# Kernel tuning notes

Measured on AMD Instinct MI355X. Metric: run time of the kernel, lower is better.

Reference implementation:

```python
import jax, jax.numpy as jnp
import numpy as np

N_EMBED = 1024
N_HEADS = 16
HEAD_SIZE = N_EMBED // N_HEADS
B, T = 4, 2048
LN_EPS = 1e-5


def _layer_norm(x, gamma, beta):
    mu = jnp.mean(x, axis=-1, keepdims=True)
    var = jnp.var(x, axis=-1, keepdims=True)
    return (x - mu) * jax.lax.rsqrt(var + LN_EPS) * gamma + beta


def setup_inputs() -> dict:
    key = jax.random.key(0)
    ks = jax.random.split(key, 12)
    s = 1.0 / np.sqrt(N_EMBED)
    sh = 1.0 / np.sqrt(4 * N_EMBED)
    return {
        "x": jax.random.normal(ks[0], (B, T, N_EMBED), jnp.float32),
        "Wk": jax.random.uniform(ks[1], (N_EMBED, N_EMBED), jnp.float32, -s, s),
        "Wq": jax.random.uniform(ks[2], (N_EMBED, N_EMBED), jnp.float32, -s, s),
        "Wv": jax.random.uniform(ks[3], (N_EMBED, N_EMBED), jnp.float32, -s, s),
        "Wproj": jax.random.uniform(ks[4], (N_EMBED, N_EMBED), jnp.float32, -s, s),
        "bproj": jax.random.uniform(ks[5], (N_EMBED,), jnp.float32, -s, s),
        "W1": jax.random.uniform(ks[6], (N_EMBED, 4 * N_EMBED), jnp.float32, -s, s),
        "b1": jax.random.uniform(ks[7], (4 * N_EMBED,), jnp.float32, -s, s),
        "W2": jax.random.uniform(ks[8], (4 * N_EMBED, N_EMBED), jnp.float32, -sh, sh),
        "b2": jax.random.uniform(ks[9], (N_EMBED,), jnp.float32, -sh, sh),
        "g1": jnp.ones((N_EMBED,), jnp.float32),
        "beta1": jnp.zeros((N_EMBED,), jnp.float32),
        "g2": jnp.ones((N_EMBED,), jnp.float32),
        "beta2": jnp.zeros((N_EMBED,), jnp.float32),
    }


def reference(x, Wk, Wq, Wv, Wproj, bproj, W1, b1, W2, b2, g1, beta1, g2, beta2):
    Bt, Tt, C = x.shape
    h = _layer_norm(x, g1, beta1)
    # project and split heads: (B, H, T, D)
    def heads(W):
        return (h @ W).reshape(Bt, Tt, N_HEADS, HEAD_SIZE).transpose(0, 2, 1, 3)
    q, k, v = heads(Wq), heads(Wk), heads(Wv)
    wei = jnp.einsum("bhtd,bhsd->bhts", q, k) / np.sqrt(HEAD_SIZE)
    causal = jnp.tril(jnp.ones((Tt, Tt), bool))
    wei = jnp.where(causal, wei, -jnp.inf)
    wei = jax.nn.softmax(wei, axis=-1)
    out = jnp.einsum("bhts,bhsd->bhtd", wei, v)
    out = out.transpose(0, 2, 1, 3).reshape(Bt, Tt, C)
    x = x + out @ Wproj + bproj
    h2 = _layer_norm(x, g2, beta2)
    ff = jax.nn.relu(h2 @ W1 + b1) @ W2 + b2
    return x + ff
```

## Files before the change

### kernel.cpp

```cpp
#include <hip/hip_runtime.h>
#include <stdint.h>

typedef __bf16 bf16x8 __attribute__((ext_vector_type(8)));
typedef float f32x4 __attribute__((ext_vector_type(4)));
typedef unsigned short u16x8 __attribute__((ext_vector_type(8)));
typedef unsigned short u16x4 __attribute__((ext_vector_type(4)));
typedef unsigned int u32x2 __attribute__((ext_vector_type(2)));
typedef float fvec4 __attribute__((ext_vector_type(4)));

__device__ __forceinline__ unsigned short f2b(float f) {
  unsigned u = __builtin_bit_cast(unsigned, f);
  return (unsigned short)((u + 0x7fffu + ((u >> 16) & 1u)) >> 16);
}

__device__ __forceinline__ bf16x8 ldfrag(const unsigned short* p) {
  return __builtin_bit_cast(bf16x8, *(const u16x8*)p);
}

__device__ __forceinline__ float fexp2(float x) {
  float r;
  asm("v_exp_f32 %0, %1" : "=v"(r) : "v"(x));
  return r;
}

__device__ __forceinline__ unsigned cvtpk(float a, float b) {
  unsigned r;
  asm("v_cvt_pk_bf16_f32 %0, %1, %2" : "=v"(r) : "v"(a), "v"(b));
  return r;
}

__device__ __forceinline__ void gload_lds16(const void* g, void* l) {
  auto gp = reinterpret_cast<const __attribute__((address_space(1))) void*>(
      reinterpret_cast<uintptr_t>(g));
  auto lp = reinterpret_cast<__attribute__((address_space(3))) void*>(
      reinterpret_cast<uintptr_t>(l));
  __builtin_amdgcn_global_load_lds(gp, lp, 16, 0, 0);
}

__global__ void transpose_cast(const float* __restrict__ W, unsigned short* __restrict__ Wt,
                               int K, int N) {
  __shared__ float tile[32][33];
  const int n0 = blockIdx.x * 32, k0 = blockIdx.y * 32;
  const int tx = threadIdx.x, ty = threadIdx.y;
#pragma unroll
  for (int j = 0; j < 4; ++j)
    tile[ty + j * 8][tx] = W[(size_t)(k0 + ty + j * 8) * N + n0 + tx];
  __syncthreads();
#pragma unroll
  for (int j = 0; j < 4; ++j)
    Wt[(size_t)(n0 + ty + j * 8) * K + k0 + tx] = f2b(tile[tx][ty + j * 8]);
}

__global__ void ln_kernel(const float* __restrict__ X, const float* __restrict__ g,
                          const float* __restrict__ be, unsigned short* __restrict__ H) {
  const int row = (blockIdx.x * blockDim.x + threadIdx.x) >> 6;
  const int l = threadIdx.x & 63;
  const float* xr = X + (size_t)row * 1024;
  fvec4 v[4];
  float s = 0.f, sq = 0.f;
#pragma unroll
  for (int i = 0; i < 4; ++i) {
    v[i] = *(const fvec4*)(xr + i * 256 + l * 4);
#pragma unroll
    for (int j = 0; j < 4; ++j) { s += v[i][j]; sq += v[i][j] * v[i][j]; }
  }
#pragma unroll
  for (int off = 32; off >= 1; off >>= 1) {
    s += __shfl_xor(s, off);
    sq += __shfl_xor(sq, off);
  }
  const float mean = s * (1.f / 1024.f);
  const float var = sq * (1.f / 1024.f) - mean * mean;
  const float rstd = rsqrtf(var + 1e-5f);
#pragma unroll
  for (int i = 0; i < 4; ++i) {
    const int col = i * 256 + l * 4;
    fvec4 gg = *(const fvec4*)(g + col);
    fvec4 bb = *(const fvec4*)(be + col);
    u16x4 o;
#pragma unroll
    for (int j = 0; j < 4; ++j) o[j] = f2b((v[i][j] - mean) * rstd * gg[j] + bb[j]);
    *(u16x4*)(H + (size_t)row * 1024 + col) = o;
  }
}

template <int BM, int BN, int WM, int WN, int NBUF, int NTH, int EPI>
__global__ __launch_bounds__(NTH, 2) void gemm8p(
    const unsigned short* __restrict__ A, const unsigned short* __restrict__ Bt,
    const float* __restrict__ bias, const float* __restrict__ resid,
    float* __restrict__ Cf, unsigned short* __restrict__ Cb,
    unsigned short* __restrict__ pK, unsigned short* __restrict__ pVT,
    int M, int N, int K, int ntiles) {
  constexpr int BK = 32;
  constexpr int ASZ = BM * BK * 2;
  constexpr int BSZ = BN * BK * 2;
  constexpr int BUFSZ = ASZ + BSZ;
  constexpr int NW = NTH / 64;
  static_assert(WM * WN == NW, "wave grid");
  constexpr int MF = BM / (WM * 16);
  constexpr int NF = BN / (WN * 16);
  constexpr int UA = ASZ / (NTH * 16);
  constexpr int UB = BSZ / (NTH * 16);
  constexpr int UNITS = UA + UB;
  constexpr int VMSTEADY = (NBUF - 2) * UNITS;
  static_assert(UA * NTH * 16 == ASZ && UB * NTH * 16 == BSZ, "unit split");
  __shared__ __align__(16) char lds[NBUF * BUFSZ];

  const int tid = threadIdx.x;
  const int w = tid >> 6, l = tid & 63;
  const int wr = w / WN, wc = w % WN;
  const int kg = l >> 4, fr = l & 15;
  const int xtiles = N / BN;
  const int nblk = (int)gridDim.x;

  int Aoff[MF], Boff[NF];
#pragma unroll
  for (int m = 0; m < MF; ++m) {
    const int r = wr * (MF * 16) + m * 16 + fr;
    Aoff[m] = r * 64 + ((kg * 16) ^ (((r >> 1) & 3) << 4));
  }
#pragma unroll
  for (int n = 0; n < NF; ++n) {
    const int r = wc * (NF * 16) + n * 16 + fr;
    Boff[n] = ASZ + r * 64 + ((kg * 16) ^ (((r >> 1) & 3) << 4));
  }

  for (int tl = (int)blockIdx.x; tl < ntiles; tl += nblk) {
    if (tl != (int)blockIdx.x) __builtin_amdgcn_s_barrier();
    const int q8 = ntiles >> 3;
    const int swz = (tl & 7) * q8 + (tl >> 3);
    const size_t am0 = (size_t)(swz / xtiles) * BM;
    const size_t bn0 = (size_t)(swz % xtiles) * BN;

    const char* src[UNITS];
#pragma unroll
    for (int u = 0; u < UA; ++u) {
      const int flatq = u * NTH + tid;
      const int row = flatq >> 2;
      const int scb = ((flatq & 3) << 4) ^ (((row >> 1) & 3) << 4);
      src[u] = (const char*)(A + (am0 + row) * K) + scb;
    }
#pragma unroll
    for (int u = 0; u < UB; ++u) {
      const int flatq = u * NTH + tid;
      const int row = flatq >> 2;
      const int scb = ((flatq & 3) << 4) ^ (((row >> 1) & 3) << 4);
      src[UA + u] = (const char*)(Bt + (bn0 + row) * K) + scb;
    }

    f32x4 acc[MF][NF];
#pragma unroll
    for (int m = 0; m < MF; ++m)
#pragma unroll
      for (int n = 0; n < NF; ++n) acc[m][n] = (f32x4){0.f, 0.f, 0.f, 0.f};

    auto stage = [&](int sb) {
#pragma unroll
      for (int u = 0; u < UNITS; ++u) {
        gload_lds16(src[u], lds + sb * BUFSZ + u * (NTH * 16) + tid * 16);
        src[u] += 64;
      }
    };

    const int NT = K / BK;
#pragma unroll
    for (int p = 0; p < NBUF - 1; ++p) stage(p);
    asm volatile("s_waitcnt vmcnt(%0)" ::"i"(VMSTEADY) : "memory");
    __builtin_amdgcn_s_barrier();

    int cb0 = 0, sb = NBUF - 1;
    for (int kt = 0; kt < NT; ++kt) {
      if (kt + NBUF - 1 < NT) stage(sb);
      bf16x8 af[MF], bf[NF];
#pragma unroll
      for (int m = 0; m < MF; ++m)
        af[m] = ldfrag((const unsigned short*)(lds + cb0 + Aoff[m]));
#pragma unroll
      for (int n = 0; n < NF; ++n)
        bf[n] = ldfrag((const unsigned short*)(lds + cb0 + Boff[n]));
      __builtin_amdgcn_s_setprio(1);
#pragma unroll
      for (int m = 0; m < MF; ++m)
#pragma unroll
        for (int n = 0; n < NF; ++n)
          acc[m][n] = __builtin_amdgcn_mfma_f32_16x16x32_bf16(af[m], bf[n], acc[m][n], 0, 0, 0);
      __builtin_amdgcn_s_setprio(0);
      if (kt + NBUF - 1 < NT) {
        asm volatile("s_waitcnt vmcnt(%0)" ::"i"(VMSTEADY) : "memory");
        __builtin_amdgcn_s_barrier();
      } else if (kt + 2 < NT) {
        asm volatile("s_waitcnt vmcnt(%0)" ::"i"(UNITS) : "memory");
        __builtin_amdgcn_s_barrier();
      } else if (kt + 1 < NT) {
        asm volatile("s_waitcnt vmcnt(0)" ::: "memory");
        __builtin_amdgcn_s_barrier();
      }
      cb0 += BUFSZ;
      if (cb0 == NBUF * BUFSZ) cb0 = 0;
      sb += 1;
      if (sb == NBUF) sb = 0;
    }

#pragma unroll
    for (int m = 0; m < MF; ++m) {
      const size_t row0 = am0 + wr * (MF * 16) + m * 16 + kg * 4;
#pragma unroll
      for (int n = 0; n < NF; ++n) {
        const size_t col = bn0 + wc * (NF * 16) + n * 16 + fr;
        if (EPI == 3) {
          if (bn0 < 1024) {
#pragma unroll
            for (int r = 0; r < 4; ++r) Cb[(row0 + r) * 1024 + col] = f2b(acc[m][n][r]);
          } else if (bn0 < 2048) {
#pragma unroll
            for (int r = 0; r < 4; ++r) pK[(row0 + r) * 1024 + col - 1024] = f2b(acc[m][n][r]);
          } else {
            const int c2 = (int)col - 2048;
            const int hh = c2 >> 6, dd = c2 & 63;
            const int bb = (int)(row0 >> 11), tt = (int)(row0 & 2047);
            u16x4 pv;
#pragma unroll
            for (int r = 0; r < 4; ++r) pv[r] = f2b(acc[m][n][r]);
            *(u16x4*)(pVT + (((size_t)bb * 16 + hh) * 64 + dd) * 2048 + tt) = pv;
          }
        } else {
          const float bv = (EPI >= 1) ? bias[col] : 0.f;
#pragma unroll
          for (int r = 0; r < 4; ++r) {
            const size_t idx = (row0 + r) * N + col;
            float v = acc[m][n][r] + bv;
            if (EPI == 1) v = fmaxf(v, 0.f);
            if (EPI == 2) {
              Cf[idx] = v + resid[idx];
            } else {
              Cb[idx] = f2b(v);
            }
          }
        }
      }
    }
  }
}

#define PSTR 72
#define SC2 0.18033688f
__global__ __launch_bounds__(256, 3) void attn_kernel(const unsigned short* __restrict__ Qb,
                                                      const unsigned short* __restrict__ Kb,
                                                      const unsigned short* __restrict__ VT,
                                                      unsigned short* __restrict__ ATT) {
  __shared__ __align__(16) char ldsK[3 * 8192];
  __shared__ __align__(16) unsigned short Pl[4][32 * PSTR];
  const int tid = threadIdx.x;
  const int w = tid >> 6, l = tid & 63;
  const int kg = l >> 4, fr = l & 15;
  const int bh = blockIdx.x;
  const int b = bh >> 4, h = bh & 15;
  const int qt = 15 - (int)blockIdx.y;
  const int q0 = qt * 128 + w * 32;
  const size_t rbase = (size_t)b * 2048;
  const unsigned short* vtb = VT + (size_t)bh * 64 * 2048;
  const f32x4 fz = {0.f, 0.f, 0.f, 0.f};

  const int rowoff = tid >> 3;
  const int cbsw = ((tid & 7) * 16) ^ ((rowoff & 7) << 4);
  const char* ksrc = (const char*)(Kb + rbase * 1024 + h * 64) + (size_t)rowoff * 2048 + cbsw;

  int koff[4][2];
#pragma unroll
  for (int sg = 0; sg < 4; ++sg)
#pragma unroll
    for (int c = 0; c < 2; ++c)
      koff[sg][c] = (sg * 16 + fr) * 128 + ((c * 64 + kg * 16) ^ ((fr & 7) << 4));

  bf16x8 bq[2][2];
#pragma unroll
  for (int qg = 0; qg < 2; ++qg) {
    const unsigned short* qrow = Qb + (rbase + q0 + qg * 16 + fr) * 1024 + h * 64;
#pragma unroll
    for (int c = 0; c < 2; ++c) bq[qg][c] = ldfrag(qrow + c * 32 + kg * 8);
  }

  f32x4 o[2][4];
#pragma unroll
  for (int qg = 0; qg < 2; ++qg)
#pragma unroll
    for (int nd = 0; nd < 4; ++nd) o[qg][nd] = (f32x4){0.f, 0.f, 0.f, 0.f};
  float m_run2[2] = {-1e30f, -1e30f}, l_run[2] = {0.f, 0.f};

  auto stage = [&](int t, int sbuf) {
    gload_lds16(ksrc + (size_t)(t * 64) * 2048, ldsK + sbuf * 8192 + tid * 16);
    gload_lds16(ksrc + (size_t)(t * 64 + 32) * 2048, ldsK + sbuf * 8192 + 4096 + tid * 16);
  };

  auto compute = [&](int s0, int cbb) {
    if (s0 > q0 + 31) return;
    bf16x8 vb[4][2];
#pragma unroll
    for (int nd = 0; nd < 4; ++nd)
#pragma unroll
      for (int ks = 0; ks < 2; ++ks)
        vb[nd][ks] = ldfrag(vtb + (size_t)(nd * 16 + fr) * 2048 + s0 + ks * 32 + kg * 8);

    f32x4 st[4][2];
#pragma unroll
    for (int sg = 0; sg < 4; ++sg) {
      const bf16x8 ka0 = ldfrag((const unsigned short*)(ldsK + cbb + koff[sg][0]));
      const bf16x8 ka1 = ldfrag((const unsigned short*)(ldsK + cbb + koff[sg][1]));
#pragma unroll
      for (int qg = 0; qg < 2; ++qg)
        st[sg][qg] = __builtin_amdgcn_mfma_f32_16x16x32_bf16(
            ka1, bq[qg][1],
            __builtin_amdgcn_mfma_f32_16x16x32_bf16(ka0, bq[qg][0], fz, 0, 0, 0), 0, 0, 0);
    }

    float psv[2];
#pragma unroll
    for (int qg = 0; qg < 2; ++qg) {
      const int qa = q0 + qg * 16 + fr;
      float vals[16];
      if (s0 + 63 <= q0 + qg * 16) {
#pragma unroll
        for (int sg = 0; sg < 4; ++sg)
#pragma unroll
          for (int r = 0; r < 4; ++r) vals[sg * 4 + r] = st[sg][qg][r];
      } else {
#pragma unroll
        for (int sg = 0; sg < 4; ++sg)
#pragma unroll
          for (int r = 0; r < 4; ++r) {
            const int sa = s0 + sg * 16 + kg * 4 + r;
            vals[sg * 4 + r] = (sa > qa) ? -1e30f : st[sg][qg][r];
          }
      }
      float m5[5];
#pragma unroll
      for (int i = 0; i < 5; ++i)
        m5[i] = fmaxf(fmaxf(vals[3 * i], vals[3 * i + 1]), vals[3 * i + 2]);
      const float vmax =
          fmaxf(fmaxf(fmaxf(m5[0], m5[1]), m5[2]), fmaxf(fmaxf(m5[3], m5[4]), vals[15]));
      const float tm2 = vmax * SC2;
      if (__any(tm2 > m_run2[qg] + 8.f)) {
        float tmax2 = tm2;
        tmax2 = fmaxf(tmax2, __shfl_xor(tmax2, 16));
        tmax2 = fmaxf(tmax2, __shfl_xor(tmax2, 32));
        const float m_new2 = fmaxf(m_run2[qg], tmax2);
        const float alpha = fexp2(m_run2[qg] - m_new2);
        m_run2[qg] = m_new2;
        l_run[qg] *= alpha;
        float al[4];
#pragma unroll
        for (int r = 0; r < 4; ++r) al[r] = __shfl(alpha, kg * 4 + r);
#pragma unroll
        for (int nd = 0; nd < 4; ++nd)
#pragma unroll
          for (int r = 0; r < 4; ++r) o[qg][nd][r] *= al[r];
      }
      const float nm2 = -m_run2[qg];
      float psum = 0.f;
      unsigned pk[8];
#pragma unroll
      for (int i = 0; i < 8; ++i) {
        const float p0 = fexp2(__builtin_fmaf(vals[2 * i], SC2, nm2));
        const float p1 = fexp2(__builtin_fmaf(vals[2 * i + 1], SC2, nm2));
        psum += p0 + p1;
        pk[i] = cvtpk(p0, p1);
      }
      psv[qg] = psum;
#pragma unroll
      for (int sg = 0; sg < 4; ++sg) {
        u32x2 w2 = {pk[2 * sg], pk[2 * sg + 1]};
        *(u32x2*)(&Pl[w][(qg * 16 + fr) * PSTR + sg * 16 + kg * 4]) = w2;
      }
    }

    {
      const float a0 = __shfl_xor(psv[0], 16);
      const float a1 = __shfl_xor(psv[1], 16);
      psv[0] += a0;
      psv[1] += a1;
      const float b0 = __shfl_xor(psv[0], 32);
      const float b1 = __shfl_xor(psv[1], 32);
      l_run[0] += psv[0] + b0;
      l_run[1] += psv[1] + b1;
    }

#pragma unroll
    for (int qg = 0; qg < 2; ++qg)
#pragma unroll
      for (int ks = 0; ks < 2; ++ks) {
        const bf16x8 pa = ldfrag(&Pl[w][(qg * 16 + fr) * PSTR + ks * 32 + kg * 8]);
#pragma unroll
        for (int nd = 0; nd < 4; ++nd)
          o[qg][nd] = __builtin_amdgcn_mfma_f32_16x16x32_bf16(pa, vb[nd][ks], o[qg][nd], 0, 0, 0);
      }
  };

  const int NT = 2 * qt + 2;
  stage(0, 0);
  stage(1, 1);
  asm volatile("s_waitcnt vmcnt(2)" ::: "memory");
  __builtin_amdgcn_s_barrier();
  int cb = 0, sb = 2;
  for (int t = 0; t < NT; ++t) {
    if (t + 2 < NT) stage(t + 2, sb);
    compute(t * 64, cb * 8192);
    if (t + 2 < NT) {
      asm volatile("s_waitcnt vmcnt(2)" ::: "memory");
      __builtin_amdgcn_s_barrier();
    } else if (t + 1 < NT) {
      asm volatile("s_waitcnt vmcnt(0)" ::: "memory");
      __builtin_amdgcn_s_barrier();
    }
    cb += 1; if (cb == 3) cb = 0;
    sb += 1; if (sb == 3) sb = 0;
  }

#pragma unroll
  for (int qg = 0; qg < 2; ++qg) {
    const float li = __builtin_amdgcn_rcpf(l_run[qg]);
    float linv[4];
#pragma unroll
    for (int r = 0; r < 4; ++r) linv[r] = __shfl(li, kg * 4 + r);
#pragma unroll
    for (int nd = 0; nd < 4; ++nd)
#pragma unroll
      for (int r = 0; r < 4; ++r) {
        const size_t row = rbase + q0 + qg * 16 + kg * 4 + r;
        ATT[row * 1024 + h * 64 + nd * 16 + fr] = f2b(o[qg][nd][r] * linv[r]);
      }
  }
}

extern "C" void kernel_launch(void* const* d_in, const int* in_sizes, int n_in, void* d_out,
                              int out_size, void* d_ws, size_t ws_size, hipStream_t stream) {
  const float* x = (const float*)d_in[0];
  const float* Wk = (const float*)d_in[1];
  const float* Wq = (const float*)d_in[2];
  const float* Wv = (const float*)d_in[3];
  const float* Wproj = (const float*)d_in[4];
  const float* bproj = (const float*)d_in[5];
  const float* W1 = (const float*)d_in[6];
  const float* b1 = (const float*)d_in[7];
  const float* W2 = (const float*)d_in[8];
  const float* b2 = (const float*)d_in[9];
  const float* g1 = (const float*)d_in[10];
  const float* beta1 = (const float*)d_in[11];
  const float* g2 = (const float*)d_in[12];
  const float* beta2 = (const float*)d_in[13];
  float* out = (float*)d_out;
  unsigned short* wsu = (unsigned short*)d_ws;

  const size_t o_qkvW = 0;
  const size_t o_projW = o_qkvW + 3072 * 1024;
  const size_t o_W1 = o_projW + 1024 * 1024;
  const size_t o_W2 = o_W1 + 4096 * 1024;
  const size_t o_H = o_W2 + 1024 * 4096;
  const size_t o_Q = o_H + (size_t)8192 * 1024;
  const size_t o_K = o_Q + (size_t)8192 * 1024;
  const size_t o_VT = o_K + (size_t)8192 * 1024;
  const size_t o_ATT = o_VT + (size_t)8192 * 1024;
  const size_t o_FF1 = o_Q;

  dim3 tpb(32, 8);
  transpose_cast<<<dim3(32, 32), tpb, 0, stream>>>(Wq, wsu + o_qkvW, 1024, 1024);
  transpose_cast<<<dim3(32, 32), tpb, 0, stream>>>(Wk, wsu + o_qkvW + 1024 * 1024, 1024, 1024);
  transpose_cast<<<dim3(32, 32), tpb, 0, stream>>>(Wv, wsu + o_qkvW + 2 * 1024 * 1024, 1024, 1024);
  transpose_cast<<<dim3(32, 32), tpb, 0, stream>>>(Wproj, wsu + o_projW, 1024, 1024);
  transpose_cast<<<dim3(128, 32), tpb, 0, stream>>>(W1, wsu + o_W1, 1024, 4096);
  transpose_cast<<<dim3(32, 128), tpb, 0, stream>>>(W2, wsu + o_W2, 4096, 1024);

  ln_kernel<<<2048, 256, 0, stream>>>(x, g1, beta1, wsu + o_H);

  gemm8p<256, 128, 2, 2, 3, 256, 3><<<512, 256, 0, stream>>>(
      wsu + o_H, wsu + o_qkvW, nullptr, nullptr, nullptr, wsu + o_Q, wsu + o_K, wsu + o_VT,
      8192, 3072, 1024, 768);

  attn_kernel<<<dim3(64, 16), 256, 0, stream>>>(wsu + o_Q, wsu + o_K, wsu + o_VT, wsu + o_ATT);

  gemm8p<128, 128, 2, 2, 3, 256, 2><<<512, 256, 0, stream>>>(
      wsu + o_ATT, wsu + o_projW, bproj, x, out, nullptr, nullptr, nullptr,
      8192, 1024, 1024, 512);

  ln_kernel<<<2048, 256, 0, stream>>>(out, g2, beta2, wsu + o_H);

  gemm8p<256, 128, 2, 2, 3, 256, 1><<<512, 256, 0, stream>>>(
      wsu + o_H, wsu + o_W1, b1, nullptr, nullptr, wsu + o_FF1, nullptr, nullptr,
      8192, 4096, 1024, 1024);

  gemm8p<128, 128, 2, 2, 3, 256, 2><<<512, 256, 0, stream>>>(
      wsu + o_FF1, wsu + o_W2, b2, out, out, nullptr, nullptr, nullptr,
      8192, 1024, 4096, 512);
}
```

Before: 356.7 us.

## Double attention query tile per block to 256 rows with 64 rows per wave

Each attention block now handles 256 query rows instead of 128, with each wave owning 64 rows (four 16-row groups). Each K tile loaded into LDS and each V fragment loaded from global memory now serves twice as many queries, which cuts K/V traffic and staging overhead per query. The grid is halved and block order is interleaved (7,6,5,4,0,1,2,3) to balance causal work. Register pressure rises, so launch bounds drop to 2 blocks per SM, and fewer, larger blocks leave a coarser load-balance tail.

```diff
diff --git a/kernel.cpp b/kernel.cpp
--- a/kernel.cpp
+++ b/kernel.cpp
@@ -244,19 +244,20 @@
 
 #define PSTR 72
 #define SC2 0.18033688f
-__global__ __launch_bounds__(256, 3) void attn_kernel(const unsigned short* __restrict__ Qb,
+__global__ __launch_bounds__(256, 2) void attn_kernel(const unsigned short* __restrict__ Qb,
                                                       const unsigned short* __restrict__ Kb,
                                                       const unsigned short* __restrict__ VT,
                                                       unsigned short* __restrict__ ATT) {
   __shared__ __align__(16) char ldsK[3 * 8192];
-  __shared__ __align__(16) unsigned short Pl[4][32 * PSTR];
+  __shared__ __align__(16) unsigned short Pl[4][64 * PSTR];
   const int tid = threadIdx.x;
   const int w = tid >> 6, l = tid & 63;
   const int kg = l >> 4, fr = l & 15;
   const int bh = blockIdx.x;
   const int b = bh >> 4, h = bh & 15;
-  const int qt = 15 - (int)blockIdx.y;
-  const int q0 = qt * 128 + w * 32;
+  const int yy = (int)blockIdx.y;
+  const int qt = (yy < 4) ? 7 - yy : yy - 4;
+  const int q0 = qt * 256 + w * 64;
   const size_t rbase = (size_t)b * 2048;
   const unsigned short* vtb = VT + (size_t)bh * 64 * 2048;
   const f32x4 fz = {0.f, 0.f, 0.f, 0.f};
@@ -272,28 +273,87 @@
     for (int c = 0; c < 2; ++c)
       koff[sg][c] = (sg * 16 + fr) * 128 + ((c * 64 + kg * 16) ^ ((fr & 7) << 4));
 
-  bf16x8 bq[2][2];
-#pragma unroll
-  for (int qg = 0; qg < 2; ++qg) {
+  bf16x8 bq[4][2];
+#pragma unroll
+  for (int qg = 0; qg < 4; ++qg) {
     const unsigned short* qrow = Qb + (rbase + q0 + qg * 16 + fr) * 1024 + h * 64;
 #pragma unroll
     for (int c = 0; c < 2; ++c) bq[qg][c] = ldfrag(qrow + c * 32 + kg * 8);
   }
 
-  f32x4 o[2][4];
-#pragma unroll
-  for (int qg = 0; qg < 2; ++qg)
+  f32x4 o[4][4];
+#pragma unroll
+  for (int qg = 0; qg < 4; ++qg)
 #pragma unroll
     for (int nd = 0; nd < 4; ++nd) o[qg][nd] = (f32x4){0.f, 0.f, 0.f, 0.f};
-  float m_run2[2] = {-1e30f, -1e30f}, l_run[2] = {0.f, 0.f};
+  float m_run2[4] = {-1e30f, -1e30f, -1e30f, -1e30f};
+  float l_run[4] = {0.f, 0.f, 0.f, 0.f};
 
   auto stage = [&](int t, int sbuf) {
     gload_lds16(ksrc + (size_t)(t * 64) * 2048, ldsK + sbuf * 8192 + tid * 16);
     gload_lds16(ksrc + (size_t)(t * 64 + 32) * 2048, ldsK + sbuf * 8192 + 4096 + tid * 16);
   };
 
+  auto softmax_qg = [&](int qg, int s0, f32x4 (&stq)[4]) -> float {
+    const int qa = q0 + qg * 16 + fr;
+    float vals[16];
+    if (s0 + 63 <= q0 + qg * 16) {
+#pragma unroll
+      for (int sg = 0; sg < 4; ++sg)
+#pragma unroll
+        for (int r = 0; r < 4; ++r) vals[sg * 4 + r] = stq[sg][r];
+    } else {
+#pragma unroll
+      for (int sg = 0; sg < 4; ++sg)
+#pragma unroll
+        for (int r = 0; r < 4; ++r) {
+          const int sa = s0 + sg * 16 + kg * 4 + r;
+          vals[sg * 4 + r] = (sa > qa) ? -1e30f : stq[sg][r];
+        }
+    }
+    float m5[5];
+#pragma unroll
+    for (int i = 0; i < 5; ++i)
+      m5[i] = fmaxf(fmaxf(vals[3 * i], vals[3 * i + 1]), vals[3 * i + 2]);
+    const float vmax =
+        fmaxf(fmaxf(fmaxf(m5[0], m5[1]), m5[2]), fmaxf(fmaxf(m5[3], m5[4]), vals[15]));
+    const float tm2 = vmax * SC2;
+    if (__any(tm2 > m_run2[qg] + 8.f)) {
+      float tmax2 = tm2;
+      tmax2 = fmaxf(tmax2, __shfl_xor(tmax2, 16));
+      tmax2 = fmaxf(tmax2, __shfl_xor(tmax2, 32));
+      const float m_new2 = fmaxf(m_run2[qg], tmax2);
+      const float alpha = fexp2(m_run2[qg] - m_new2);
+      m_run2[qg] = m_new2;
+      l_run[qg] *= alpha;
+      float al[4];
+#pragma unroll
+      for (int r = 0; r < 4; ++r) al[r] = __shfl(alpha, kg * 4 + r);
+#pragma unroll
+      for (int nd = 0; nd < 4; ++nd)
+#pragma unroll
+        for (int r = 0; r < 4; ++r) o[qg][nd][r] *= al[r];
+    }
+    const float nm2 = -m_run2[qg];
+    float psum = 0.f;
+    unsigned pk[8];
+#pragma unroll
+    for (int i = 0; i < 8; ++i) {
+      const float p0 = fexp2(__builtin_fmaf(vals[2 * i], SC2, nm2));
+      const float p1 = fexp2(__builtin_fmaf(vals[2 * i + 1], SC2, nm2));
+      psum += p0 + p1;
+      pk[i] = cvtpk(p0, p1);
+    }
+#pragma unroll
+    for (int sg = 0; sg < 4; ++sg) {
+      u32x2 w2 = {pk[2 * sg], pk[2 * sg + 1]};
+      *(u32x2*)(&Pl[w][(qg * 16 + fr) * PSTR + sg * 16 + kg * 4]) = w2;
+    }
+    return psum;
+  };
+
   auto compute = [&](int s0, int cbb) {
-    if (s0 > q0 + 31) return;
+    if (s0 > q0 + 63) return;
     bf16x8 vb[4][2];
 #pragma unroll
     for (int nd = 0; nd < 4; ++nd)
@@ -301,91 +361,44 @@
       for (int ks = 0; ks < 2; ++ks)
         vb[nd][ks] = ldfrag(vtb + (size_t)(nd * 16 + fr) * 2048 + s0 + ks * 32 + kg * 8);
 
-    f32x4 st[4][2];
-#pragma unroll
-    for (int sg = 0; sg < 4; ++sg) {
-      const bf16x8 ka0 = ldfrag((const unsigned short*)(ldsK + cbb + koff[sg][0]));
-      const bf16x8 ka1 = ldfrag((const unsigned short*)(ldsK + cbb + koff[sg][1]));
-#pragma unroll
-      for (int qg = 0; qg < 2; ++qg)
-        st[sg][qg] = __builtin_amdgcn_mfma_f32_16x16x32_bf16(
-            ka1, bq[qg][1],
-            __builtin_amdgcn_mfma_f32_16x16x32_bf16(ka0, bq[qg][0], fz, 0, 0, 0), 0, 0, 0);
-    }
-
-    float psv[2];
-#pragma unroll
-    for (int qg = 0; qg < 2; ++qg) {
-      const int qa = q0 + qg * 16 + fr;
-      float vals[16];
-      if (s0 + 63 <= q0 + qg * 16) {
-#pragma unroll
-        for (int sg = 0; sg < 4; ++sg)
-#pragma unroll
-          for (int r = 0; r < 4; ++r) vals[sg * 4 + r] = st[sg][qg][r];
-      } else {
-#pragma unroll
-        for (int sg = 0; sg < 4; ++sg)
-#pragma unroll
-          for (int r = 0; r < 4; ++r) {
-            const int sa = s0 + sg * 16 + kg * 4 + r;
-            vals[sg * 4 + r] = (sa > qa) ? -1e30f : st[sg][qg][r];
-          }
-      }
-      float m5[5];
-#pragma unroll
-      for (int i = 0; i < 5; ++i)
-        m5[i] = fmaxf(fmaxf(vals[3 * i], vals[3 * i + 1]), vals[3 * i + 2]);
-      const float vmax =
-          fmaxf(fmaxf(fmaxf(m5[0], m5[1]), m5[2]), fmaxf(fmaxf(m5[3], m5[4]), vals[15]));
-      const float tm2 = vmax * SC2;
-      if (__any(tm2 > m_run2[qg] + 8.f)) {
-        float tmax2 = tm2;
-        tmax2 = fmaxf(tmax2, __shfl_xor(tmax2, 16));
-        tmax2 = fmaxf(tmax2, __shfl_xor(tmax2, 32));
-        const float m_new2 = fmaxf(m_run2[qg], tmax2);
-        const float alpha = fexp2(m_run2[qg] - m_new2);
-        m_run2[qg] = m_new2;
-        l_run[qg] *= alpha;
-        float al[4];
-#pragma unroll
-        for (int r = 0; r < 4; ++r) al[r] = __shfl(alpha, kg * 4 + r);
-#pragma unroll
-        for (int nd = 0; nd < 4; ++nd)
-#pragma unroll
-          for (int r = 0; r < 4; ++r) o[qg][nd][r] *= al[r];
-      }
-      const float nm2 = -m_run2[qg];
-      float psum = 0.f;
-      unsigned pk[8];
-#pragma unroll
-      for (int i = 0; i < 8; ++i) {
-        const float p0 = fexp2(__builtin_fmaf(vals[2 * i], SC2, nm2));
-        const float p1 = fexp2(__builtin_fmaf(vals[2 * i + 1], SC2, nm2));
-        psum += p0 + p1;
-        pk[i] = cvtpk(p0, p1);
-      }
-      psv[qg] = psum;
+    float psv[4];
+#pragma unroll
+    for (int qp = 0; qp < 2; ++qp) {
+      f32x4 st[4][2];
 #pragma unroll
       for (int sg = 0; sg < 4; ++sg) {
-        u32x2 w2 = {pk[2 * sg], pk[2 * sg + 1]};
-        *(u32x2*)(&Pl[w][(qg * 16 + fr) * PSTR + sg * 16 + kg * 4]) = w2;
+        const bf16x8 ka0 = ldfrag((const unsigned short*)(ldsK + cbb + koff[sg][0]));
+        const bf16x8 ka1 = ldfrag((const unsigned short*)(ldsK + cbb + koff[sg][1]));
+#pragma unroll
+        for (int qh = 0; qh < 2; ++qh)
+          st[sg][qh] = __builtin_amdgcn_mfma_f32_16x16x32_bf16(
+              ka1, bq[qp * 2 + qh][1],
+              __builtin_amdgcn_mfma_f32_16x16x32_bf16(ka0, bq[qp * 2 + qh][0], fz, 0, 0, 0),
+              0, 0, 0);
+      }
+#pragma unroll
+      for (int qh = 0; qh < 2; ++qh) {
+        f32x4 stq[4];
+#pragma unroll
+        for (int sg = 0; sg < 4; ++sg) stq[sg] = st[sg][qh];
+        psv[qp * 2 + qh] = softmax_qg(qp * 2 + qh, s0, stq);
       }
     }
 
     {
-      const float a0 = __shfl_xor(psv[0], 16);
-      const float a1 = __shfl_xor(psv[1], 16);
-      psv[0] += a0;
-      psv[1] += a1;
-      const float b0 = __shfl_xor(psv[0], 32);
-      const float b1 = __shfl_xor(psv[1], 32);
-      l_run[0] += psv[0] + b0;
-      l_run[1] += psv[1] + b1;
-    }
-
-#pragma unroll
-    for (int qg = 0; qg < 2; ++qg)
+      float a[4], c[4];
+#pragma unroll
+      for (int qg = 0; qg < 4; ++qg) a[qg] = __shfl_xor(psv[qg], 16);
+#pragma unroll
+      for (int qg = 0; qg < 4; ++qg) psv[qg] += a[qg];
+#pragma unroll
+      for (int qg = 0; qg < 4; ++qg) c[qg] = __shfl_xor(psv[qg], 32);
+#pragma unroll
+      for (int qg = 0; qg < 4; ++qg) l_run[qg] += psv[qg] + c[qg];
+    }
+
+#pragma unroll
+    for (int qg = 0; qg < 4; ++qg)
 #pragma unroll
       for (int ks = 0; ks < 2; ++ks) {
         const bf16x8 pa = ldfrag(&Pl[w][(qg * 16 + fr) * PSTR + ks * 32 + kg * 8]);
@@ -395,7 +408,7 @@
       }
   };
 
-  const int NT = 2 * qt + 2;
+  const int NT = 4 * qt + 4;
   stage(0, 0);
   stage(1, 1);
   asm volatile("s_waitcnt vmcnt(2)" ::: "memory");
@@ -416,7 +429,7 @@
   }
 
 #pragma unroll
-  for (int qg = 0; qg < 2; ++qg) {
+  for (int qg = 0; qg < 4; ++qg) {
     const float li = __builtin_amdgcn_rcpf(l_run[qg]);
     float linv[4];
 #pragma unroll
@@ -475,7 +488,7 @@
       wsu + o_H, wsu + o_qkvW, nullptr, nullptr, nullptr, wsu + o_Q, wsu + o_K, wsu + o_VT,
       8192, 3072, 1024, 768);
 
-  attn_kernel<<<dim3(64, 16), 256, 0, stream>>>(wsu + o_Q, wsu + o_K, wsu + o_VT, wsu + o_ATT);
+  attn_kernel<<<dim3(64, 8), 256, 0, stream>>>(wsu + o_Q, wsu + o_K, wsu + o_VT, wsu + o_ATT);
 
   gemm8p<128, 128, 2, 2, 3, 256, 2><<<512, 256, 0, stream>>>(
       wsu + o_ATT, wsu + o_projW, bproj, x, out, nullptr, nullptr, nullptr,
```

Result: no change. 351.5 us (-1.5%).
